# Optimization experiments

Measured on AMD Instinct MI355X. Metric: run time of the kernel, lower is better.

## Reference

```python
import jax, jax.numpy as jnp
import numpy as np

NUM_EXPERTS = 8
TOP_K = 2
HIDDEN = 1024
INTER = 4096
STD = 0.02


def setup_inputs() -> dict:
    key = jax.random.key(0)
    k0, k1, k2, k3 = jax.random.split(key, 4)
    hidden_states = jax.random.normal(k0, (2, 2048, HIDDEN), dtype=jnp.float32)
    gate_w = jax.random.normal(k1, (NUM_EXPERTS, HIDDEN), dtype=jnp.float32) * (HIDDEN ** -0.5)
    w1 = jax.random.normal(k2, (NUM_EXPERTS, INTER, HIDDEN), dtype=jnp.float32) * STD  # c_fc.weight
    w2 = jax.random.normal(k3, (NUM_EXPERTS, HIDDEN, INTER), dtype=jnp.float32) * STD  # c_proj.weight
    return {"hidden_states": hidden_states, "gate_w": gate_w, "w1": w1, "w2": w2}


def reference(hidden_states, gate_w, w1, w2):
    B, S, H = hidden_states.shape
    x = hidden_states.reshape(-1, H)                      # [T, H]
    T = x.shape[0]
    # ---- routing ----
    router_logits = x @ gate_w.T                          # [T, E]
    top_vals, top_idx = jax.lax.top_k(router_logits, TOP_K)
    router_weights = jax.nn.softmax(top_vals.astype(jnp.float32), axis=-1).astype(x.dtype)
    # dense combine matrix with exactly top_k nonzeros per row (math-equivalent
    # to the sort/grouped-GEMM/scatter-combine pipeline in the torch module)
    combine = jnp.zeros((T, NUM_EXPERTS), x.dtype).at[
        jnp.arange(T)[:, None], top_idx
    ].set(router_weights)                                 # [T, E]
    # ---- experts ----
    h = jax.nn.gelu(jnp.einsum('th,eih->eti', x, w1), approximate=False)  # [E, T, I]
    y = jnp.einsum('eti,ehi->eth', h, w2)                 # [E, T, H]
    out = jnp.einsum('eth,te->th', y, combine)            # weighted combine
    return out.reshape(B, S, H), router_logits
```

## Files before the change

### kernel.cpp

```cpp
#include <hip/hip_runtime.h>

#define T 4096
#define Hdim 1024
#define Idim 4096
#define NE 8
#define OUT0 4194304

#define SLOT_CAP 9216

#define W1B_OFF 0u
#define W2B_OFF 67108864u
#define XB_OFF  134217728u
#define HB_OFF  142606336u
#define YB_OFF  218103808u
#define META_OFF 255852544u
#define M_COUNTS 0
#define M_CURS   8
#define M_OFFS   16
#define M_TEXP   32
#define M_TSLOT  8224
#define M_STOK   16416
#define M_TWF    25632

typedef short bf16x8 __attribute__((ext_vector_type(8)));
typedef float f32x4  __attribute__((ext_vector_type(4)));

__device__ __forceinline__ unsigned short f2bf(float f) {
    unsigned int b = __float_as_uint(f);
    b += 0x7fffu + ((b >> 16) & 1u);
    return (unsigned short)(b >> 16);
}

__device__ __forceinline__ void gl_lds16(const void* g, void* l) {
    __builtin_amdgcn_global_load_lds((const __attribute__((address_space(1))) void*)g,
                                     (__attribute__((address_space(3))) void*)l,
                                     16, 0, 0);
}

__global__ void zero_meta_k(int* meta) {
    int i = blockIdx.x * blockDim.x + threadIdx.x;
    if (i < 16) meta[i] = 0;
    if (i < SLOT_CAP) meta[M_STOK + i] = -1;
}

__global__ void cvt_bf16_k(const float* __restrict__ src, unsigned short* __restrict__ dst, int n4) {
    int i = blockIdx.x * blockDim.x + threadIdx.x;
    if (i >= n4) return;
    float4 v = ((const float4*)src)[i];
    ushort4 o;
    o.x = f2bf(v.x); o.y = f2bf(v.y); o.z = f2bf(v.z); o.w = f2bf(v.w);
    ((ushort4*)dst)[i] = o;
}

__global__ void router_k(const float* __restrict__ x, const float* __restrict__ gw,
                         float* __restrict__ logits_out, int* __restrict__ texp,
                         float* __restrict__ twf, int* __restrict__ counts) {
    int wv = threadIdx.x >> 6, lane = threadIdx.x & 63;
    int t = blockIdx.x * 4 + wv;
    const float* xp = x + (size_t)t * Hdim;
    float s[NE];
    #pragma unroll
    for (int e = 0; e < NE; e++) s[e] = 0.f;
    #pragma unroll
    for (int j = 0; j < 16; j++) {
        float xv = xp[lane + 64 * j];
        #pragma unroll
        for (int e = 0; e < NE; e++) s[e] += xv * gw[e * Hdim + lane + 64 * j];
    }
    #pragma unroll
    for (int e = 0; e < NE; e++) {
        #pragma unroll
        for (int off = 32; off > 0; off >>= 1) s[e] += __shfl_xor(s[e], off);
    }
    if (lane == 0) {
        #pragma unroll
        for (int e = 0; e < NE; e++) logits_out[t * NE + e] = s[e];
        int i0 = 0; float v0 = s[0];
        #pragma unroll
        for (int e = 1; e < NE; e++) if (s[e] > v0) { v0 = s[e]; i0 = e; }
        int i1 = -1; float v1 = -3.4e38f;
        #pragma unroll
        for (int e = 0; e < NE; e++) if (e != i0 && s[e] > v1) { v1 = s[e]; i1 = e; }
        float e1 = __expf(v1 - v0) ;
        e1 = expf(v1 - v0);
        float inv = 1.f / (1.f + e1);
        texp[2 * t] = i0; texp[2 * t + 1] = i1;
        twf[2 * t] = inv; twf[2 * t + 1] = e1 * inv;
        atomicAdd(&counts[i0], 1);
        atomicAdd(&counts[i1], 1);
    }
}

__global__ void offsets_k(const int* __restrict__ counts, int* __restrict__ offs) {
    if (threadIdx.x == 0 && blockIdx.x == 0) {
        int a = 0; offs[0] = 0;
        for (int e = 0; e < NE; e++) { a += (counts[e] + 127) & ~127; offs[e + 1] = a; }
    }
}

__global__ void assign_k(const int* __restrict__ texp, const int* __restrict__ offs,
                         int* __restrict__ curs, int* __restrict__ stok, int* __restrict__ tslot) {
    int p = blockIdx.x * blockDim.x + threadIdx.x;
    int e = texp[p];
    int slot = offs[e] + atomicAdd(&curs[e], 1);
    stok[slot] = p >> 1;
    tslot[p] = slot;
}

__global__ __launch_bounds__(256) void gemm1_k(
    const unsigned short* __restrict__ xb, const unsigned short* __restrict__ w1b,
    const int* __restrict__ offs, const int* __restrict__ stok,
    unsigned short* __restrict__ hb) {
    __shared__ __align__(16) unsigned short As[128 * 32];
    __shared__ __align__(16) unsigned short Bs[128 * 32];
    const int rt = blockIdx.y, ct = blockIdx.x;
    const int row0 = rt * 128;
    if (row0 >= offs[NE]) return;
    int e = 0;
    #pragma unroll
    for (int q = 1; q < NE; q++) if (offs[q] <= row0) e = q;

    const int tid = threadIdx.x;
    const int lane = tid & 63, wv = tid >> 6;
    const int c0 = wv * 2, c1 = wv * 2 + 1;
    const int rin = lane >> 2, kc = lane & 3;
    const int ar0 = c0 * 16 + rin, ar1 = c1 * 16 + rin;
    int t0 = stok[row0 + ar0]; if (t0 < 0) t0 = 0;
    int t1 = stok[row0 + ar1]; if (t1 < 0) t1 = 0;
    const unsigned short* gA0 = xb + (size_t)t0 * Hdim + kc * 8;
    const unsigned short* gA1 = xb + (size_t)t1 * Hdim + kc * 8;
    const unsigned short* gB0 = w1b + ((size_t)e * Idim + ct * 128 + ar0) * Hdim + kc * 8;
    const unsigned short* gB1 = w1b + ((size_t)e * Idim + ct * 128 + ar1) * Hdim + kc * 8;
    unsigned short* lA0 = As + c0 * 512; unsigned short* lA1 = As + c1 * 512;
    unsigned short* lB0 = Bs + c0 * 512; unsigned short* lB1 = Bs + c1 * 512;

    f32x4 acc[4][4] = {};
    const int mrow = (wv & 1) * 64, ncol = (wv >> 1) * 64;
    const int fr = lane & 15, qd = lane >> 4;

    for (int kk = 0; kk < Hdim; kk += 32) {
        gl_lds16(gA0 + kk, lA0);
        gl_lds16(gA1 + kk, lA1);
        gl_lds16(gB0 + kk, lB0);
        gl_lds16(gB1 + kk, lB1);
        __syncthreads();
        bf16x8 af[4], bff[4];
        #pragma unroll
        for (int mi = 0; mi < 4; mi++) af[mi]  = *(const bf16x8*)&As[(mrow + mi * 16 + fr) * 32 + qd * 8];
        #pragma unroll
        for (int ni = 0; ni < 4; ni++) bff[ni] = *(const bf16x8*)&Bs[(ncol + ni * 16 + fr) * 32 + qd * 8];
        #pragma unroll
        for (int mi = 0; mi < 4; mi++)
            #pragma unroll
            for (int ni = 0; ni < 4; ni++)
                acc[mi][ni] = __builtin_amdgcn_mfma_f32_16x16x32_bf16(af[mi], bff[ni], acc[mi][ni], 0, 0, 0);
        __syncthreads();
    }
    #pragma unroll
    for (int mi = 0; mi < 4; mi++) {
        #pragma unroll
        for (int ni = 0; ni < 4; ni++) {
            #pragma unroll
            for (int r = 0; r < 4; r++) {
                int row = row0 + mrow + mi * 16 + qd * 4 + r;
                int col = ct * 128 + ncol + ni * 16 + fr;
                float v = acc[mi][ni][r];
                float g = 0.5f * v * (1.f + erff(v * 0.70710678f));
                hb[(size_t)row * Idim + col] = f2bf(g);
            }
        }
    }
}

__global__ __launch_bounds__(256) void gemm2_k(
    const unsigned short* __restrict__ hb, const unsigned short* __restrict__ w2b,
    const int* __restrict__ offs, float* __restrict__ yb) {
    __shared__ __align__(16) unsigned short As[128 * 32];
    __shared__ __align__(16) unsigned short Bs[128 * 32];
    const int rt = blockIdx.y, ct = blockIdx.x;
    const int row0 = rt * 128;
    if (row0 >= offs[NE]) return;
    int e = 0;
    #pragma unroll
    for (int q = 1; q < NE; q++) if (offs[q] <= row0) e = q;

    const int tid = threadIdx.x;
    const int lane = tid & 63, wv = tid >> 6;
    const int c0 = wv * 2, c1 = wv * 2 + 1;
    const int rin = lane >> 2, kc = lane & 3;
    const int ar0 = c0 * 16 + rin, ar1 = c1 * 16 + rin;
    const unsigned short* gA0 = hb + (size_t)(row0 + ar0) * Idim + kc * 8;
    const unsigned short* gA1 = hb + (size_t)(row0 + ar1) * Idim + kc * 8;
    const unsigned short* gB0 = w2b + ((size_t)e * Hdim + ct * 128 + ar0) * Idim + kc * 8;
    const unsigned short* gB1 = w2b + ((size_t)e * Hdim + ct * 128 + ar1) * Idim + kc * 8;
    unsigned short* lA0 = As + c0 * 512; unsigned short* lA1 = As + c1 * 512;
    unsigned short* lB0 = Bs + c0 * 512; unsigned short* lB1 = Bs + c1 * 512;

    f32x4 acc[4][4] = {};
    const int mrow = (wv & 1) * 64, ncol = (wv >> 1) * 64;
    const int fr = lane & 15, qd = lane >> 4;

    for (int kk = 0; kk < Idim; kk += 32) {
        gl_lds16(gA0 + kk, lA0);
        gl_lds16(gA1 + kk, lA1);
        gl_lds16(gB0 + kk, lB0);
        gl_lds16(gB1 + kk, lB1);
        __syncthreads();
        bf16x8 af[4], bff[4];
        #pragma unroll
        for (int mi = 0; mi < 4; mi++) af[mi]  = *(const bf16x8*)&As[(mrow + mi * 16 + fr) * 32 + qd * 8];
        #pragma unroll
        for (int ni = 0; ni < 4; ni++) bff[ni] = *(const bf16x8*)&Bs[(ncol + ni * 16 + fr) * 32 + qd * 8];
        #pragma unroll
        for (int mi = 0; mi < 4; mi++)
            #pragma unroll
            for (int ni = 0; ni < 4; ni++)
                acc[mi][ni] = __builtin_amdgcn_mfma_f32_16x16x32_bf16(af[mi], bff[ni], acc[mi][ni], 0, 0, 0);
        __syncthreads();
    }
    #pragma unroll
    for (int mi = 0; mi < 4; mi++) {
        #pragma unroll
        for (int ni = 0; ni < 4; ni++) {
            #pragma unroll
            for (int r = 0; r < 4; r++) {
                int row = row0 + mrow + mi * 16 + qd * 4 + r;
                int col = ct * 128 + ncol + ni * 16 + fr;
                yb[(size_t)row * Hdim + col] = acc[mi][ni][r];
            }
        }
    }
}

__global__ void combine_k(const float* __restrict__ yb, const int* __restrict__ tslot,
                          const float* __restrict__ twf, float* __restrict__ out) {
    int i = blockIdx.x * blockDim.x + threadIdx.x;
    int t = i >> 8, rem = i & 255;
    int s0 = tslot[2 * t], s1 = tslot[2 * t + 1];
    float w0 = twf[2 * t], w1 = twf[2 * t + 1];
    float4 a = ((const float4*)yb)[(size_t)s0 * 256 + rem];
    float4 b = ((const float4*)yb)[(size_t)s1 * 256 + rem];
    float4 o;
    o.x = w0 * a.x + w1 * b.x;
    o.y = w0 * a.y + w1 * b.y;
    o.z = w0 * a.z + w1 * b.z;
    o.w = w0 * a.w + w1 * b.w;
    ((float4*)out)[i] = o;
}

extern "C" void kernel_launch(void* const* d_in, const int* in_sizes, int n_in,
                              void* d_out, int out_size, void* d_ws, size_t ws_size,
                              hipStream_t stream) {
    const float* x  = (const float*)d_in[0];
    const float* gw = (const float*)d_in[1];
    const float* w1 = (const float*)d_in[2];
    const float* w2 = (const float*)d_in[3];
    float* out = (float*)d_out;

    char* ws = (char*)d_ws;
    unsigned short* w1b = (unsigned short*)(ws + W1B_OFF);
    unsigned short* w2b = (unsigned short*)(ws + W2B_OFF);
    unsigned short* xb  = (unsigned short*)(ws + XB_OFF);
    unsigned short* hb  = (unsigned short*)(ws + HB_OFF);
    float*          yb  = (float*)(ws + YB_OFF);
    int*            meta = (int*)(ws + META_OFF);
    int* counts = meta + M_COUNTS;
    int* curs   = meta + M_CURS;
    int* offs   = meta + M_OFFS;
    int* texp   = meta + M_TEXP;
    int* tslot  = meta + M_TSLOT;
    int* stok   = meta + M_STOK;
    float* twf  = (float*)(meta + M_TWF);

    zero_meta_k<<<36, 256, 0, stream>>>(meta);
    cvt_bf16_k<<<4096, 256, 0, stream>>>(x, xb, T * Hdim / 4);
    cvt_bf16_k<<<32768, 256, 0, stream>>>(w1, w1b, NE * Idim * Hdim / 4);
    cvt_bf16_k<<<32768, 256, 0, stream>>>(w2, w2b, NE * Hdim * Idim / 4);
    router_k<<<T / 4, 256, 0, stream>>>(x, gw, out + OUT0, texp, twf, counts);
    offsets_k<<<1, 64, 0, stream>>>(counts, offs);
    assign_k<<<32, 256, 0, stream>>>(texp, offs, curs, stok, tslot);
    gemm1_k<<<dim3(Idim / 128, SLOT_CAP / 128), 256, 0, stream>>>(xb, w1b, offs, stok, hb);
    gemm2_k<<<dim3(Hdim / 128, SLOT_CAP / 128), 256, 0, stream>>>(hb, w2b, offs, yb);
    combine_k<<<T * Hdim / 4 / 256, 256, 0, stream>>>(yb, tslot, twf, out);
}
```

Before: 770.4 us.

## Split-K gemm2 with atomic accumulation, fuse weight and x bf16 conversions

Measured after the change: 778.0 us. No clear change (+1.0%).

```diff
diff --git a/kernel.cpp b/kernel.cpp
--- a/kernel.cpp
+++ b/kernel.cpp
@@ -5,6 +5,7 @@
 #define Idim 4096
 #define NE 8
 #define OUT0 4194304
+#define SPLITK 4
 
 #define SLOT_CAP 9216
 
@@ -22,6 +23,8 @@
 #define M_STOK   16416
 #define M_TWF    25632
 
+#define NY4 (SLOT_CAP * Hdim / 4)
+
 typedef short bf16x8 __attribute__((ext_vector_type(8)));
 typedef float f32x4  __attribute__((ext_vector_type(4)));
 
@@ -37,33 +40,41 @@
                                      16, 0, 0);
 }
 
-__global__ void zero_meta_k(int* meta) {
+__global__ void zero_k(int* meta, float4* y4) {
     int i = blockIdx.x * blockDim.x + threadIdx.x;
+    if (i < NY4) y4[i] = make_float4(0.f, 0.f, 0.f, 0.f);
     if (i < 16) meta[i] = 0;
     if (i < SLOT_CAP) meta[M_STOK + i] = -1;
 }
 
-__global__ void cvt_bf16_k(const float* __restrict__ src, unsigned short* __restrict__ dst, int n4) {
+__global__ void cvt_w_k(const float* __restrict__ w1, const float* __restrict__ w2,
+                        unsigned short* __restrict__ w1b, unsigned short* __restrict__ w2b,
+                        int n4each) {
     int i = blockIdx.x * blockDim.x + threadIdx.x;
-    if (i >= n4) return;
-    float4 v = ((const float4*)src)[i];
+    const float4* src; ushort4* dst; int j;
+    if (i < n4each) { src = (const float4*)w1; dst = (ushort4*)w1b; j = i; }
+    else            { src = (const float4*)w2; dst = (ushort4*)w2b; j = i - n4each; }
+    float4 v = src[j];
     ushort4 o;
     o.x = f2bf(v.x); o.y = f2bf(v.y); o.z = f2bf(v.z); o.w = f2bf(v.w);
-    ((ushort4*)dst)[i] = o;
+    dst[j] = o;
 }
 
 __global__ void router_k(const float* __restrict__ x, const float* __restrict__ gw,
                          float* __restrict__ logits_out, int* __restrict__ texp,
-                         float* __restrict__ twf, int* __restrict__ counts) {
+                         float* __restrict__ twf, int* __restrict__ counts,
+                         unsigned short* __restrict__ xb) {
     int wv = threadIdx.x >> 6, lane = threadIdx.x & 63;
     int t = blockIdx.x * 4 + wv;
     const float* xp = x + (size_t)t * Hdim;
+    unsigned short* xbp = xb + (size_t)t * Hdim;
     float s[NE];
     #pragma unroll
     for (int e = 0; e < NE; e++) s[e] = 0.f;
     #pragma unroll
     for (int j = 0; j < 16; j++) {
         float xv = xp[lane + 64 * j];
+        xbp[lane + 64 * j] = f2bf(xv);
         #pragma unroll
         for (int e = 0; e < NE; e++) s[e] += xv * gw[e * Hdim + lane + 64 * j];
     }
@@ -81,8 +92,7 @@
         int i1 = -1; float v1 = -3.4e38f;
         #pragma unroll
         for (int e = 0; e < NE; e++) if (e != i0 && s[e] > v1) { v1 = s[e]; i1 = e; }
-        float e1 = __expf(v1 - v0) ;
-        e1 = expf(v1 - v0);
+        float e1 = expf(v1 - v0);
         float inv = 1.f / (1.f + e1);
         texp[2 * t] = i0; texp[2 * t + 1] = i1;
         twf[2 * t] = inv; twf[2 * t + 1] = e1 * inv;
@@ -177,7 +187,7 @@
     const int* __restrict__ offs, float* __restrict__ yb) {
     __shared__ __align__(16) unsigned short As[128 * 32];
     __shared__ __align__(16) unsigned short Bs[128 * 32];
-    const int rt = blockIdx.y, ct = blockIdx.x;
+    const int rt = blockIdx.y, ct = blockIdx.x, kz = blockIdx.z;
     const int row0 = rt * 128;
     if (row0 >= offs[NE]) return;
     int e = 0;
@@ -200,7 +210,8 @@
     const int mrow = (wv & 1) * 64, ncol = (wv >> 1) * 64;
     const int fr = lane & 15, qd = lane >> 4;
 
-    for (int kk = 0; kk < Idim; kk += 32) {
+    const int k0 = kz * (Idim / SPLITK), k1 = k0 + (Idim / SPLITK);
+    for (int kk = k0; kk < k1; kk += 32) {
         gl_lds16(gA0 + kk, lA0);
         gl_lds16(gA1 + kk, lA1);
         gl_lds16(gB0 + kk, lB0);
@@ -226,7 +237,7 @@
             for (int r = 0; r < 4; r++) {
                 int row = row0 + mrow + mi * 16 + qd * 4 + r;
                 int col = ct * 128 + ncol + ni * 16 + fr;
-                yb[(size_t)row * Hdim + col] = acc[mi][ni][r];
+                unsafeAtomicAdd(&yb[(size_t)row * Hdim + col], acc[mi][ni][r]);
             }
         }
     }
@@ -272,14 +283,12 @@
     int* stok   = meta + M_STOK;
     float* twf  = (float*)(meta + M_TWF);
 
-    zero_meta_k<<<36, 256, 0, stream>>>(meta);
-    cvt_bf16_k<<<4096, 256, 0, stream>>>(x, xb, T * Hdim / 4);
-    cvt_bf16_k<<<32768, 256, 0, stream>>>(w1, w1b, NE * Idim * Hdim / 4);
-    cvt_bf16_k<<<32768, 256, 0, stream>>>(w2, w2b, NE * Hdim * Idim / 4);
-    router_k<<<T / 4, 256, 0, stream>>>(x, gw, out + OUT0, texp, twf, counts);
+    zero_k<<<NY4 / 256 + 1, 256, 0, stream>>>(meta, (float4*)yb);
+    cvt_w_k<<<65536, 256, 0, stream>>>(w1, w2, w1b, w2b, NE * Idim * Hdim / 4);
+    router_k<<<T / 4, 256, 0, stream>>>(x, gw, out + OUT0, texp, twf, counts, xb);
     offsets_k<<<1, 64, 0, stream>>>(counts, offs);
     assign_k<<<32, 256, 0, stream>>>(texp, offs, curs, stok, tslot);
     gemm1_k<<<dim3(Idim / 128, SLOT_CAP / 128), 256, 0, stream>>>(xb, w1b, offs, stok, hb);
-    gemm2_k<<<dim3(Hdim / 128, SLOT_CAP / 128), 256, 0, stream>>>(hb, w2b, offs, yb);
+    gemm2_k<<<dim3(Hdim / 128, SLOT_CAP / 128, SPLITK), 256, 0, stream>>>(hb, w2b, offs, yb);
     combine_k<<<T * Hdim / 4 / 256, 256, 0, stream>>>(yb, tslot, twf, out);
 }
```
